# Kernel optimization log

Measured on AMD Instinct MI355X. Metric: run time of the kernel, lower is better.

Reference implementation:

```python
import jax, jax.numpy as jnp
import numpy as np

N = 50000       # nodes
E = 800000      # edges (avg degree 16)
IN = 256        # input feature dim
HID = 64        # per-head hidden dim
H = 2           # heads
C = 64          # num_classes (final single-head layer width)
NEG_SLOPE = 0.01  # torch F.leaky_relu default


def setup_inputs() -> dict:
    key = jax.random.key(0)
    ks = jax.random.split(key, 24)
    nrm = lambda k, shape, scale: jax.random.normal(k, shape, jnp.float32) * scale
    features = nrm(ks[0], (N, IN), 1.0)
    src = jax.random.randint(ks[1], (E,), 0, N)
    dst = jax.random.randint(ks[2], (E,), 0, N)
    # layer 0: H heads, Linear(IN->HID) + attn_l/attn_r Linear(HID->1)
    W0 = nrm(ks[3], (H, IN, HID), IN ** -0.5)
    b0 = jnp.zeros((H, HID), jnp.float32)
    al0 = nrm(ks[4], (H, HID), HID ** -0.5)
    bl0 = jnp.zeros((H,), jnp.float32)
    ar0 = nrm(ks[5], (H, HID), HID ** -0.5)
    br0 = jnp.zeros((H,), jnp.float32)
    # layer 1: H heads, Linear(H*HID->HID)
    W1 = nrm(ks[6], (H, H * HID, HID), (H * HID) ** -0.5)
    b1 = jnp.zeros((H, HID), jnp.float32)
    al1 = nrm(ks[7], (H, HID), HID ** -0.5)
    bl1 = jnp.zeros((H,), jnp.float32)
    ar1 = nrm(ks[8], (H, HID), HID ** -0.5)
    br1 = jnp.zeros((H,), jnp.float32)
    # final: 1 head, Linear(H*HID->C)
    Wf = nrm(ks[9], (1, H * HID, C), (H * HID) ** -0.5)
    bf = jnp.zeros((1, C), jnp.float32)
    alf = nrm(ks[10], (1, C), C ** -0.5)
    blf = jnp.zeros((1,), jnp.float32)
    arf = nrm(ks[11], (1, C), C ** -0.5)
    brf = jnp.zeros((1,), jnp.float32)
    return dict(features=features, src=src, dst=dst,
                W0=W0, b0=b0, al0=al0, bl0=bl0, ar0=ar0, br0=br0,
                W1=W1, b1=b1, al1=al1, bl1=bl1, ar1=ar1, br1=br1,
                Wf=Wf, bf=bf, alf=alf, blf=blf, arf=arf, brf=brf)


def gat_layer(x, src, dst, W, b, al, bl, ar, br):
    # x: [N, D]; W: [H, D, K]
    ft = jnp.einsum('nd,hdk->nhk', x, W) + b          # [N,H,K]
    a1 = jnp.einsum('nhk,hk->nh', ft, al) + bl        # [N,H] (dst-side)
    a2 = jnp.einsum('nhk,hk->nh', ft, ar) + br        # [N,H] (src-side)
    s = jax.nn.leaky_relu(a1[dst] + a2[src], NEG_SLOPE)  # [E,H]
    m = jax.ops.segment_max(s, dst, num_segments=N)      # per-dst max for stable softmax
    e = jnp.exp(s - m[dst])
    denom = jax.ops.segment_sum(e, dst, num_segments=N)
    alpha = e / denom[dst]                               # edge softmax over in-neighbors
    accum = jax.ops.segment_sum(alpha[:, :, None] * ft[src], dst, num_segments=N)  # [N,H,K]
    return jax.nn.elu(accum)


def reference(features, src, dst,
              W0, b0, al0, bl0, ar0, br0,
              W1, b1, al1, bl1, ar1, br1,
              Wf, bf, alf, blf, arf, brf):
    x = gat_layer(features, src, dst, W0, b0, al0, bl0, ar0, br0).reshape(N, H * HID)
    x = gat_layer(x, src, dst, W1, b1, al1, bl1, ar1, br1).reshape(N, H * HID)
    out = gat_layer(x, src, dst, Wf, bf, alf, blf, arf, brf)[:, 0, :]  # [N,C]
    return out
```

## Files before the change

### kernel.cpp

```cpp
#include <hip/hip_runtime.h>
#include <math.h>

#define NN 50000
#define EE 800000
#define DIN 256
#define NEG_SLOPE 0.01f
#define CAPSH 7
#define CAP (1 << CAPSH)

typedef __attribute__((ext_vector_type(8))) short bf16x8;
typedef __attribute__((ext_vector_type(8))) unsigned short u16x8;
typedef __attribute__((ext_vector_type(4))) float f32x4;

__device__ __forceinline__ unsigned short bf16_rne(float f) {
    unsigned int u = __float_as_uint(f);
    u += 0x7fffu + ((u >> 16) & 1u);
    return (unsigned short)(u >> 16);
}
__device__ __forceinline__ float bf16_tof(unsigned short h) {
    return __uint_as_float(((unsigned int)h) << 16);
}

__device__ __forceinline__ void fmamix_lo(float& a, unsigned f, float w) {
    asm("v_fma_mix_f32 %0, %1, %2, %0 op_sel:[0,0,0] op_sel_hi:[1,0,0]"
        : "+v"(a)
        : "v"(f), "v"(w));
}
__device__ __forceinline__ void fmamix_hi(float& a, unsigned f, float w) {
    asm("v_fma_mix_f32 %0, %1, %2, %0 op_sel:[1,0,0] op_sel_hi:[1,0,0]"
        : "+v"(a)
        : "v"(f), "v"(w));
}

__global__ __launch_bounds__(256) void scatter_kernel(const int* __restrict__ src,
                                                      const int* __restrict__ dst,
                                                      const int* __restrict__ pos,
                                                      int* __restrict__ esrc, int E) {
    int e = blockIdx.x * 256 + threadIdx.x;
    if (e >= E) return;
    int p = pos[e];
    if (p < CAP) esrc[(dst[e] << CAPSH) + p] = src[e];
}

__global__ __launch_bounds__(256) void conv_w_kernel(
    const float* __restrict__ W0, const float* __restrict__ W1,
    const float* __restrict__ Wf, unsigned short* __restrict__ w0h,
    unsigned short* __restrict__ w0l, unsigned short* __restrict__ w1h,
    unsigned short* __restrict__ w1l, unsigned short* __restrict__ wfh,
    unsigned short* __restrict__ wfl, int* __restrict__ cnt) {
    int t = blockIdx.x * 256 + threadIdx.x;
    const float* W;
    unsigned short *oh, *ol;
    int D, u;
    if (t < 32768) { W = W0; oh = w0h; ol = w0l; D = 256; u = t; }
    else if (t < 49152) { W = W1; oh = w1h; ol = w1l; D = 128; u = t - 32768; }
    else if (t < 57344) { W = Wf; oh = wfh; ol = wfl; D = 128; u = t - 49152; }
    else {
        int c = t - 57344;
        if (c < NN) cnt[c] = 0;
        return;
    }
    int d = u & (D - 1);
    int n = u / D;
    float v = W[((size_t)(n >> 6) * D + d) * 64 + (n & 63)];
    unsigned short hi = bf16_rne(v);
    unsigned short lo = bf16_rne(v - bf16_tof(hi));
    oh[(size_t)n * D + d] = hi;
    ol[(size_t)n * D + d] = lo;
}

#define LDK 40

template <int NCOL, bool AFP32, bool HIST>
__global__ __launch_bounds__(256) void gemm_attn(
    const float* __restrict__ Xf, const unsigned short* __restrict__ Xhi,
    const unsigned short* __restrict__ Xlo, const unsigned short* __restrict__ Wthi,
    const unsigned short* __restrict__ Wtlo, const float* __restrict__ bias,
    const float* __restrict__ al, const float* __restrict__ bl,
    const float* __restrict__ ar, const float* __restrict__ br,
    _Float16* __restrict__ FT, float* __restrict__ A1, float* __restrict__ A2,
    int Nn, int D, const int* __restrict__ edst, int* __restrict__ cnt,
    int* __restrict__ pos, int E, int gemmBlocks) {
    if (HIST) {
        if ((int)blockIdx.x >= gemmBlocks) {
            int e = ((int)blockIdx.x - gemmBlocks) * 256 + threadIdx.x;
            if (e < E) pos[e] = atomicAdd(&cnt[edst[e]], 1);
            return;
        }
    }
    const int H = NCOL / 64;
    const int NC16 = NCOL / 16;
    __shared__ __align__(16) unsigned short Ahi_s[64 * LDK];
    __shared__ __align__(16) unsigned short Alo_s[64 * LDK];
    __shared__ __align__(16) unsigned short Bhi_s[NCOL * LDK];
    __shared__ __align__(16) unsigned short Blo_s[NCOL * LDK];

    int tid = threadIdx.x;
    int wv = tid >> 6, l = tid & 63, lm = l & 15, quad = l >> 4;
    int m0 = blockIdx.x * 64;

    f32x4 acc[NC16];
#pragma unroll
    for (int c = 0; c < NC16; c++) acc[c] = (f32x4){0.f, 0.f, 0.f, 0.f};

    for (int d0 = 0; d0 < D; d0 += 32) {
        if (AFP32) {
#pragma unroll
            for (int i = 0; i < 2; i++) {
                int u = tid + i * 256;
                int row = u >> 3, c4 = u & 7;
                float4 v = make_float4(0.f, 0.f, 0.f, 0.f);
                if (m0 + row < Nn)
                    v = *(const float4*)&Xf[(size_t)(m0 + row) * D + d0 + c4 * 4];
                float f[4] = {v.x, v.y, v.z, v.w};
                unsigned short hi[4], lo[4];
#pragma unroll
                for (int j = 0; j < 4; j++) {
                    hi[j] = bf16_rne(f[j]);
                    lo[j] = bf16_rne(f[j] - bf16_tof(hi[j]));
                }
                *(ushort4*)&Ahi_s[row * LDK + c4 * 4] = make_ushort4(hi[0], hi[1], hi[2], hi[3]);
                *(ushort4*)&Alo_s[row * LDK + c4 * 4] = make_ushort4(lo[0], lo[1], lo[2], lo[3]);
            }
        } else {
            int row = tid >> 2, q = tid & 3;
            u16x8 vh = (u16x8)0, vl = (u16x8)0;
            if (m0 + row < Nn) {
                vh = *(const u16x8*)&Xhi[(size_t)(m0 + row) * D + d0 + q * 8];
                vl = *(const u16x8*)&Xlo[(size_t)(m0 + row) * D + d0 + q * 8];
            }
            *(u16x8*)&Ahi_s[row * LDK + q * 8] = vh;
            *(u16x8*)&Alo_s[row * LDK + q * 8] = vl;
        }
#pragma unroll
        for (int i = 0; i < NCOL / 64; i++) {
            int u = tid + i * 256;
            int n = u >> 2, q = u & 3;
            *(u16x8*)&Bhi_s[n * LDK + q * 8] =
                *(const u16x8*)&Wthi[(size_t)n * D + d0 + q * 8];
            *(u16x8*)&Blo_s[n * LDK + q * 8] =
                *(const u16x8*)&Wtlo[(size_t)n * D + d0 + q * 8];
        }
        __syncthreads();

        int arow = wv * 16 + lm;
        bf16x8 ah = *(const bf16x8*)&Ahi_s[arow * LDK + quad * 8];
        bf16x8 alo = *(const bf16x8*)&Alo_s[arow * LDK + quad * 8];
#pragma unroll
        for (int cg = 0; cg < NC16; cg += 4) {
            bf16x8 bh4[4], bl4[4];
#pragma unroll
            for (int u = 0; u < 4; u++) {
                bh4[u] = *(const bf16x8*)&Bhi_s[((cg + u) * 16 + lm) * LDK + quad * 8];
                bl4[u] = *(const bf16x8*)&Blo_s[((cg + u) * 16 + lm) * LDK + quad * 8];
            }
#pragma unroll
            for (int u = 0; u < 4; u++)
                acc[cg + u] = __builtin_amdgcn_mfma_f32_16x16x32_bf16(ah, bh4[u], acc[cg + u], 0, 0, 0);
#pragma unroll
            for (int u = 0; u < 4; u++)
                acc[cg + u] = __builtin_amdgcn_mfma_f32_16x16x32_bf16(ah, bl4[u], acc[cg + u], 0, 0, 0);
#pragma unroll
            for (int u = 0; u < 4; u++)
                acc[cg + u] = __builtin_amdgcn_mfma_f32_16x16x32_bf16(alo, bh4[u], acc[cg + u], 0, 0, 0);
        }
        __syncthreads();
    }

    float bj[NC16], alj[NC16], arj[NC16];
#pragma unroll
    for (int c = 0; c < NC16; c++) {
        bj[c] = bias[c * 16 + lm];
        alj[c] = al[c * 16 + lm];
        arj[c] = ar[c * 16 + lm];
    }
#pragma unroll
    for (int reg = 0; reg < 4; reg++) {
        int row = m0 + wv * 16 + quad * 4 + reg;
        bool ok = row < Nn;
        float s1[H], s2[H];
#pragma unroll
        for (int h = 0; h < H; h++) { s1[h] = 0.f; s2[h] = 0.f; }
#pragma unroll
        for (int c = 0; c < NC16; c++) {
            float o = acc[c][reg] + bj[c];
            int h = c >> 2;
            s1[h] += o * alj[c];
            s2[h] += o * arj[c];
            if (ok) FT[(size_t)row * NCOL + c * 16 + lm] = (_Float16)o;
        }
#pragma unroll
        for (int h = 0; h < H; h++) {
#pragma unroll
            for (int d = 1; d < 16; d <<= 1) {
                s1[h] += __shfl_xor(s1[h], d);
                s2[h] += __shfl_xor(s2[h], d);
            }
        }
        if (ok && lm == 0) {
#pragma unroll
            for (int h = 0; h < H; h++) {
                A1[(size_t)row * H + h] = s1[h] + bl[h];
                A2[(size_t)row * H + h] = s2[h] + br[h];
            }
        }
    }
}

__global__ __launch_bounds__(256) void agg2_kernel(
    const _Float16* __restrict__ ft, const float* __restrict__ a1,
    const float* __restrict__ a2, const int* __restrict__ cnt,
    const int* __restrict__ esrc, unsigned short* __restrict__ ohi,
    unsigned short* __restrict__ olo, int Nn) {
    __shared__ __align__(16) int2 pk0s[4][64];
    __shared__ __align__(16) int2 pk1s[4][64];
    int wv = threadIdx.x >> 6, lane = threadIdx.x & 63;
    int n = blockIdx.x * 4 + wv;
    if (n >= Nn) return;
    int o0 = n << CAPSH, deg = cnt[n];
    int hs = lane >> 5, cl2 = lane * 2;
    unsigned lb = (unsigned)lane * 4u;
    if (deg == 0) {
        *(ushort2*)&ohi[(size_t)n * 128 + cl2] = make_ushort2(0, 0);
        *(ushort2*)&olo[(size_t)n * 128 + cl2] = make_ushort2(0, 0);
        return;
    }
    const char* ftb = (const char*)ft;
    const int2* pw = hs ? pk1s[wv] : pk0s[wv];
    float2 a1v = *(const float2*)&a1[(size_t)n * 2];
    float ax = 0.f, ay = 0.f;
    float ds0 = 0.f, ds1 = 0.f;
    for (int e0 = 0; e0 < deg; e0 += 64) {
        int nE = min(64, deg - e0);
        float w0 = 0.f, w1 = 0.f;
        int sj = 0;
        if (lane < nE) {
            sj = esrc[o0 + e0 + lane];
            float2 a2j = *(const float2*)((const char*)a2 + ((unsigned)sj << 3));
            float t0 = a1v.x + a2j.x;
            float t1 = a1v.y + a2j.y;
            t0 = t0 > 0.f ? t0 : NEG_SLOPE * t0;
            t1 = t1 > 0.f ? t1 : NEG_SLOPE * t1;
            w0 = __expf(t0);
            w1 = __expf(t1);
        }
        ds0 += w0;
        ds1 += w1;
        pk0s[wv][lane] = make_int2(sj, __float_as_int(w0));
        pk1s[wv][lane] = make_int2(sj, __float_as_int(w1));
        int nB = (nE + 15) >> 4;
        for (int b = 0; b < nB; b++) {
            int j = b * 16;
            int2 pb[16];
#pragma unroll
            for (int u = 0; u < 16; u++) pb[u] = pw[j + u];
            unsigned f[16];
#pragma unroll
            for (int u = 0; u < 16; u++)
                f[u] = *(const unsigned*)(ftb + (((unsigned)pb[u].x << 8) + lb));
#pragma unroll
            for (int u = 0; u < 16; u++) {
                float w = __int_as_float(pb[u].y);
                fmamix_lo(ax, f[u], w);
                fmamix_hi(ay, f[u], w);
            }
        }
    }
#pragma unroll
    for (int d = 1; d < 64; d <<= 1) {
        ds0 += __shfl_xor(ds0, d);
        ds1 += __shfl_xor(ds1, d);
    }
    float rd = 1.f / (hs ? ds1 : ds0);
    float rx = ax * rd, ry = ay * rd;
    rx = rx > 0.f ? rx : expm1f(rx);
    ry = ry > 0.f ? ry : expm1f(ry);
    unsigned short hx = bf16_rne(rx), hy = bf16_rne(ry);
    unsigned short lx = bf16_rne(rx - bf16_tof(hx)), ly = bf16_rne(ry - bf16_tof(hy));
    *(ushort2*)&ohi[(size_t)n * 128 + cl2] = make_ushort2(hx, hy);
    *(ushort2*)&olo[(size_t)n * 128 + cl2] = make_ushort2(lx, ly);
}

__global__ __launch_bounds__(256) void agg1_kernel(
    const _Float16* __restrict__ ft, const float* __restrict__ a1,
    const float* __restrict__ a2, const int* __restrict__ cnt,
    const int* __restrict__ esrc, float* __restrict__ out, int Nn) {
    __shared__ __align__(16) int2 pks[4][64];
    int wv = threadIdx.x >> 6, lane = threadIdx.x & 63;
    int n = blockIdx.x * 4 + wv;
    if (n >= Nn) return;
    int o0 = n << CAPSH, deg = cnt[n];
    if (deg == 0) {
        out[(size_t)n * 64 + lane] = 0.f;
        return;
    }
    const char* ftb = (const char*)ft;
    unsigned lb = (unsigned)lane * 2u;
    float a1v = a1[n];
    float acc = 0.f, dsum = 0.f;
    for (int e0 = 0; e0 < deg; e0 += 64) {
        int nE = min(64, deg - e0);
        float wl = 0.f;
        int sj = 0;
        if (lane < nE) {
            sj = esrc[o0 + e0 + lane];
            float t = a1v + a2[sj];
            t = t > 0.f ? t : NEG_SLOPE * t;
            wl = __expf(t);
        }
        dsum += wl;
        pks[wv][lane] = make_int2(sj, __float_as_int(wl));
        int nB = (nE + 15) >> 4;
        for (int b = 0; b < nB; b++) {
            int j = b * 16;
            int2 pb[16];
#pragma unroll
            for (int u = 0; u < 16; u++) pb[u] = pks[wv][j + u];
            unsigned f[16];
#pragma unroll
            for (int u = 0; u < 16; u++)
                f[u] = *(const unsigned short*)(ftb + (((unsigned)pb[u].x << 7) + lb));
#pragma unroll
            for (int u = 0; u < 16; u++)
                fmamix_lo(acc, f[u], __int_as_float(pb[u].y));
        }
    }
#pragma unroll
    for (int d = 1; d < 64; d <<= 1) dsum += __shfl_xor(dsum, d);
    float r = acc / dsum;
    out[(size_t)n * 64 + lane] = r > 0.f ? r : expm1f(r);
}

extern "C" void kernel_launch(void* const* d_in, const int* in_sizes, int n_in,
                              void* d_out, int out_size, void* d_ws, size_t ws_size,
                              hipStream_t stream) {
    const float* features = (const float*)d_in[0];
    const int* src = (const int*)d_in[1];
    const int* dst = (const int*)d_in[2];
    const float* W0 = (const float*)d_in[3];
    const float* b0 = (const float*)d_in[4];
    const float* al0 = (const float*)d_in[5];
    const float* bl0 = (const float*)d_in[6];
    const float* ar0 = (const float*)d_in[7];
    const float* br0 = (const float*)d_in[8];
    const float* W1 = (const float*)d_in[9];
    const float* b1 = (const float*)d_in[10];
    const float* al1 = (const float*)d_in[11];
    const float* bl1 = (const float*)d_in[12];
    const float* ar1 = (const float*)d_in[13];
    const float* br1 = (const float*)d_in[14];
    const float* Wf = (const float*)d_in[15];
    const float* bf = (const float*)d_in[16];
    const float* alf = (const float*)d_in[17];
    const float* blf = (const float*)d_in[18];
    const float* arf = (const float*)d_in[19];
    const float* brf = (const float*)d_in[20];

    char* p = (char*)d_ws;
    auto carve = [&](size_t bytes) {
        void* q = (void*)p;
        p += (bytes + 255) & ~(size_t)255;
        return q;
    };
    _Float16* ft = (_Float16*)carve((size_t)NN * 128 * 2);
    unsigned short* Xhi = (unsigned short*)carve((size_t)NN * 128 * 2);
    unsigned short* Xlo = (unsigned short*)carve((size_t)NN * 128 * 2);
    float* a1 = (float*)carve((size_t)NN * 2 * 4);
    float* a2 = (float*)carve((size_t)NN * 2 * 4);
    int* cnt = (int*)carve((size_t)NN * 4);
    int* pos = (int*)carve((size_t)EE * 4);
    int* esrc = (int*)carve((size_t)NN * CAP * 4);
    unsigned short* w0h = (unsigned short*)carve(32768 * 2);
    unsigned short* w0l = (unsigned short*)carve(32768 * 2);
    unsigned short* w1h = (unsigned short*)carve(16384 * 2);
    unsigned short* w1l = (unsigned short*)carve(16384 * 2);
    unsigned short* wfh = (unsigned short*)carve(8192 * 2);
    unsigned short* wfl = (unsigned short*)carve(8192 * 2);

    const int GE = (EE + 255) / 256;
    const int gx = (NN + 63) / 64;
    const int gn = (NN + 3) / 4;

    conv_w_kernel<<<(57344 + NN + 255) / 256, 256, 0, stream>>>(
        W0, W1, Wf, w0h, w0l, w1h, w1l, wfh, wfl, cnt);

    gemm_attn<128, true, true><<<gx + GE, 256, 0, stream>>>(
        features, nullptr, nullptr, w0h, w0l, b0, al0, bl0, ar0, br0, ft, a1, a2,
        NN, DIN, dst, cnt, pos, EE, gx);

    scatter_kernel<<<GE, 256, 0, stream>>>(src, dst, pos, esrc, EE);

    agg2_kernel<<<gn, 256, 0, stream>>>(ft, a1, a2, cnt, esrc, Xhi, Xlo, NN);

    gemm_attn<128, false, false><<<gx, 256, 0, stream>>>(
        nullptr, Xhi, Xlo, w1h, w1l, b1, al1, bl1, ar1, br1, ft, a1, a2, NN, 128,
        nullptr, nullptr, nullptr, 0, 0);
    agg2_kernel<<<gn, 256, 0, stream>>>(ft, a1, a2, cnt, esrc, Xhi, Xlo, NN);

    gemm_attn<64, false, false><<<gx, 256, 0, stream>>>(
        nullptr, Xhi, Xlo, wfh, wfl, bf, alf, blf, arf, brf, ft, a1, a2, NN, 128,
        nullptr, nullptr, nullptr, 0, 0);
    agg1_kernel<<<gn, 256, 0, stream>>>(ft, a1, a2, cnt, esrc, (float*)d_out, NN);
}
```

Before: 292.0 us.

## Fuse edge aggregation with next layer GEMM, keeping aggregated tile in LDS

Merges the layer aggregation kernel with the following layer's projection GEMM. Each block aggregates 64 destination nodes into a swizzled LDS tile of bf16 hi/lo values, then multiplies that tile by the next weight matrix with MFMA. This removes the global write and re-read of the Xhi/Xlo intermediate and two kernel launches. Block count drops from one wave per node across many blocks to 64 nodes per block, which reduces parallelism and latency hiding for the irregular gather phase. Double-buffered ft/a1/a2 buffers are added to avoid read/write aliasing.

```diff
diff --git a/kernel.cpp b/kernel.cpp
--- a/kernel.cpp
+++ b/kernel.cpp
@@ -71,25 +71,20 @@
 
 #define LDK 40
 
-template <int NCOL, bool AFP32, bool HIST>
-__global__ __launch_bounds__(256) void gemm_attn(
-    const float* __restrict__ Xf, const unsigned short* __restrict__ Xhi,
-    const unsigned short* __restrict__ Xlo, const unsigned short* __restrict__ Wthi,
+__global__ __launch_bounds__(256) void gemm0_kernel(
+    const float* __restrict__ Xf, const unsigned short* __restrict__ Wthi,
     const unsigned short* __restrict__ Wtlo, const float* __restrict__ bias,
     const float* __restrict__ al, const float* __restrict__ bl,
     const float* __restrict__ ar, const float* __restrict__ br,
     _Float16* __restrict__ FT, float* __restrict__ A1, float* __restrict__ A2,
     int Nn, int D, const int* __restrict__ edst, int* __restrict__ cnt,
     int* __restrict__ pos, int E, int gemmBlocks) {
-    if (HIST) {
-        if ((int)blockIdx.x >= gemmBlocks) {
-            int e = ((int)blockIdx.x - gemmBlocks) * 256 + threadIdx.x;
-            if (e < E) pos[e] = atomicAdd(&cnt[edst[e]], 1);
-            return;
-        }
-    }
-    const int H = NCOL / 64;
-    const int NC16 = NCOL / 16;
+    if ((int)blockIdx.x >= gemmBlocks) {
+        int e = ((int)blockIdx.x - gemmBlocks) * 256 + threadIdx.x;
+        if (e < E) pos[e] = atomicAdd(&cnt[edst[e]], 1);
+        return;
+    }
+    const int NCOL = 128, NC16 = 8, H = 2;
     __shared__ __align__(16) unsigned short Ahi_s[64 * LDK];
     __shared__ __align__(16) unsigned short Alo_s[64 * LDK];
     __shared__ __align__(16) unsigned short Bhi_s[NCOL * LDK];
@@ -104,36 +99,25 @@
     for (int c = 0; c < NC16; c++) acc[c] = (f32x4){0.f, 0.f, 0.f, 0.f};
 
     for (int d0 = 0; d0 < D; d0 += 32) {
-        if (AFP32) {
-#pragma unroll
-            for (int i = 0; i < 2; i++) {
-                int u = tid + i * 256;
-                int row = u >> 3, c4 = u & 7;
-                float4 v = make_float4(0.f, 0.f, 0.f, 0.f);
-                if (m0 + row < Nn)
-                    v = *(const float4*)&Xf[(size_t)(m0 + row) * D + d0 + c4 * 4];
-                float f[4] = {v.x, v.y, v.z, v.w};
-                unsigned short hi[4], lo[4];
-#pragma unroll
-                for (int j = 0; j < 4; j++) {
-                    hi[j] = bf16_rne(f[j]);
-                    lo[j] = bf16_rne(f[j] - bf16_tof(hi[j]));
-                }
-                *(ushort4*)&Ahi_s[row * LDK + c4 * 4] = make_ushort4(hi[0], hi[1], hi[2], hi[3]);
-                *(ushort4*)&Alo_s[row * LDK + c4 * 4] = make_ushort4(lo[0], lo[1], lo[2], lo[3]);
-            }
-        } else {
-            int row = tid >> 2, q = tid & 3;
-            u16x8 vh = (u16x8)0, vl = (u16x8)0;
-            if (m0 + row < Nn) {
-                vh = *(const u16x8*)&Xhi[(size_t)(m0 + row) * D + d0 + q * 8];
-                vl = *(const u16x8*)&Xlo[(size_t)(m0 + row) * D + d0 + q * 8];
-            }
-            *(u16x8*)&Ahi_s[row * LDK + q * 8] = vh;
-            *(u16x8*)&Alo_s[row * LDK + q * 8] = vl;
-        }
-#pragma unroll
-        for (int i = 0; i < NCOL / 64; i++) {
+#pragma unroll
+        for (int i = 0; i < 2; i++) {
+            int u = tid + i * 256;
+            int row = u >> 3, c4 = u & 7;
+            float4 v = make_float4(0.f, 0.f, 0.f, 0.f);
+            if (m0 + row < Nn)
+                v = *(const float4*)&Xf[(size_t)(m0 + row) * D + d0 + c4 * 4];
+            float f[4] = {v.x, v.y, v.z, v.w};
+            unsigned short hi[4], lo[4];
+#pragma unroll
+            for (int j = 0; j < 4; j++) {
+                hi[j] = bf16_rne(f[j]);
+                lo[j] = bf16_rne(f[j] - bf16_tof(hi[j]));
+            }
+            *(ushort4*)&Ahi_s[row * LDK + c4 * 4] = make_ushort4(hi[0], hi[1], hi[2], hi[3]);
+            *(ushort4*)&Alo_s[row * LDK + c4 * 4] = make_ushort4(lo[0], lo[1], lo[2], lo[3]);
+        }
+#pragma unroll
+        for (int i = 0; i < 2; i++) {
             int u = tid + i * 256;
             int n = u >> 2, q = u & 3;
             *(u16x8*)&Bhi_s[n * LDK + q * 8] =
@@ -207,78 +191,181 @@
     }
 }
 
-__global__ __launch_bounds__(256) void agg2_kernel(
-    const _Float16* __restrict__ ft, const float* __restrict__ a1,
-    const float* __restrict__ a2, const int* __restrict__ cnt,
-    const int* __restrict__ esrc, unsigned short* __restrict__ ohi,
-    unsigned short* __restrict__ olo, int Nn) {
-    __shared__ __align__(16) int2 pk0s[4][64];
-    __shared__ __align__(16) int2 pk1s[4][64];
-    int wv = threadIdx.x >> 6, lane = threadIdx.x & 63;
-    int n = blockIdx.x * 4 + wv;
-    if (n >= Nn) return;
-    int o0 = n << CAPSH, deg = cnt[n];
-    int hs = lane >> 5, cl2 = lane * 2;
-    unsigned lb = (unsigned)lane * 4u;
-    if (deg == 0) {
-        *(ushort2*)&ohi[(size_t)n * 128 + cl2] = make_ushort2(0, 0);
-        *(ushort2*)&olo[(size_t)n * 128 + cl2] = make_ushort2(0, 0);
-        return;
-    }
-    const char* ftb = (const char*)ft;
-    const int2* pw = hs ? pk1s[wv] : pk0s[wv];
-    float2 a1v = *(const float2*)&a1[(size_t)n * 2];
-    float ax = 0.f, ay = 0.f;
-    float ds0 = 0.f, ds1 = 0.f;
-    for (int e0 = 0; e0 < deg; e0 += 64) {
-        int nE = min(64, deg - e0);
-        float w0 = 0.f, w1 = 0.f;
-        int sj = 0;
-        if (lane < nE) {
-            sj = esrc[o0 + e0 + lane];
-            float2 a2j = *(const float2*)((const char*)a2 + ((unsigned)sj << 3));
-            float t0 = a1v.x + a2j.x;
-            float t1 = a1v.y + a2j.y;
-            t0 = t0 > 0.f ? t0 : NEG_SLOPE * t0;
-            t1 = t1 > 0.f ? t1 : NEG_SLOPE * t1;
-            w0 = __expf(t0);
-            w1 = __expf(t1);
-        }
-        ds0 += w0;
-        ds1 += w1;
-        pk0s[wv][lane] = make_int2(sj, __float_as_int(w0));
-        pk1s[wv][lane] = make_int2(sj, __float_as_int(w1));
-        int nB = (nE + 15) >> 4;
-        for (int b = 0; b < nB; b++) {
-            int j = b * 16;
-            int2 pb[16];
-#pragma unroll
-            for (int u = 0; u < 16; u++) pb[u] = pw[j + u];
-            unsigned f[16];
-#pragma unroll
-            for (int u = 0; u < 16; u++)
-                f[u] = *(const unsigned*)(ftb + (((unsigned)pb[u].x << 8) + lb));
-#pragma unroll
-            for (int u = 0; u < 16; u++) {
-                float w = __int_as_float(pb[u].y);
-                fmamix_lo(ax, f[u], w);
-                fmamix_hi(ay, f[u], w);
-            }
-        }
-    }
-#pragma unroll
-    for (int d = 1; d < 64; d <<= 1) {
-        ds0 += __shfl_xor(ds0, d);
-        ds1 += __shfl_xor(ds1, d);
-    }
-    float rd = 1.f / (hs ? ds1 : ds0);
-    float rx = ax * rd, ry = ay * rd;
-    rx = rx > 0.f ? rx : expm1f(rx);
-    ry = ry > 0.f ? ry : expm1f(ry);
-    unsigned short hx = bf16_rne(rx), hy = bf16_rne(ry);
-    unsigned short lx = bf16_rne(rx - bf16_tof(hx)), ly = bf16_rne(ry - bf16_tof(hy));
-    *(ushort2*)&ohi[(size_t)n * 128 + cl2] = make_ushort2(hx, hy);
-    *(ushort2*)&olo[(size_t)n * 128 + cl2] = make_ushort2(lx, ly);
+template <int NCOL>
+__global__ __launch_bounds__(256) void agg_gemm_kernel(
+    const _Float16* __restrict__ ftin, const float* __restrict__ a1in,
+    const float* __restrict__ a2in, const int* __restrict__ cnt,
+    const int* __restrict__ esrc, const unsigned short* __restrict__ Wthi,
+    const unsigned short* __restrict__ Wtlo, const float* __restrict__ bias,
+    const float* __restrict__ al, const float* __restrict__ bl,
+    const float* __restrict__ ar, const float* __restrict__ br,
+    _Float16* __restrict__ FT, float* __restrict__ A1, float* __restrict__ A2,
+    int Nn) {
+    const int NC16 = NCOL / 16;
+    const int H = NCOL / 64;
+    __shared__ __align__(16) unsigned short Ahi_t[64 * 128];
+    __shared__ __align__(16) unsigned short Alo_t[64 * 128];
+    __shared__ __align__(16) unsigned short Bhi_s[64 * LDK];
+    __shared__ __align__(16) unsigned short Blo_s[64 * LDK];
+    int2* pk0s = (int2*)Bhi_s;
+    int2* pk1s = (int2*)Blo_s;
+
+    int tid = threadIdx.x;
+    int wv = tid >> 6, lane = tid & 63, lm = lane & 15, quad = lane >> 4;
+    int m0 = blockIdx.x * 64;
+    const char* ftb = (const char*)ftin;
+
+    {
+        int hs = lane >> 5;
+        unsigned lb = (unsigned)lane * 4u;
+        const int2* pw = (hs ? pk1s : pk0s) + wv * 64;
+        for (int i = 0; i < 16; i++) {
+            int r = wv * 16 + i;
+            int n = m0 + r;
+            unsigned abyte = ((unsigned)(r * 256 + lane * 4)) ^ ((unsigned)(r & 7) << 4);
+            if (n >= Nn) {
+                *(ushort2*)((char*)Ahi_t + abyte) = make_ushort2(0, 0);
+                *(ushort2*)((char*)Alo_t + abyte) = make_ushort2(0, 0);
+                continue;
+            }
+            int deg = cnt[n];
+            if (deg == 0) {
+                *(ushort2*)((char*)Ahi_t + abyte) = make_ushort2(0, 0);
+                *(ushort2*)((char*)Alo_t + abyte) = make_ushort2(0, 0);
+                continue;
+            }
+            int o0 = n << CAPSH;
+            float2 a1v = *(const float2*)&a1in[(size_t)n * 2];
+            float ax = 0.f, ay = 0.f, ds0 = 0.f, ds1 = 0.f;
+            for (int e0 = 0; e0 < deg; e0 += 64) {
+                int nE = min(64, deg - e0);
+                float w0 = 0.f, w1 = 0.f;
+                int sj = 0;
+                if (lane < nE) {
+                    sj = esrc[o0 + e0 + lane];
+                    float2 a2j = *(const float2*)((const char*)a2in + ((unsigned)sj << 3));
+                    float t0 = a1v.x + a2j.x;
+                    float t1 = a1v.y + a2j.y;
+                    t0 = t0 > 0.f ? t0 : NEG_SLOPE * t0;
+                    t1 = t1 > 0.f ? t1 : NEG_SLOPE * t1;
+                    w0 = __expf(t0);
+                    w1 = __expf(t1);
+                }
+                ds0 += w0;
+                ds1 += w1;
+                pk0s[wv * 64 + lane] = make_int2(sj, __float_as_int(w0));
+                pk1s[wv * 64 + lane] = make_int2(sj, __float_as_int(w1));
+                int nB = (nE + 15) >> 4;
+                for (int b = 0; b < nB; b++) {
+                    int j = b * 16;
+                    int2 pb[16];
+#pragma unroll
+                    for (int u = 0; u < 16; u++) pb[u] = pw[j + u];
+                    unsigned f[16];
+#pragma unroll
+                    for (int u = 0; u < 16; u++)
+                        f[u] = *(const unsigned*)(ftb + (((unsigned)pb[u].x << 8) + lb));
+#pragma unroll
+                    for (int u = 0; u < 16; u++) {
+                        float w = __int_as_float(pb[u].y);
+                        fmamix_lo(ax, f[u], w);
+                        fmamix_hi(ay, f[u], w);
+                    }
+                }
+            }
+#pragma unroll
+            for (int d = 1; d < 64; d <<= 1) {
+                ds0 += __shfl_xor(ds0, d);
+                ds1 += __shfl_xor(ds1, d);
+            }
+            float rd = 1.f / (hs ? ds1 : ds0);
+            float rx = ax * rd, ry = ay * rd;
+            rx = rx > 0.f ? rx : expm1f(rx);
+            ry = ry > 0.f ? ry : expm1f(ry);
+            unsigned short hx = bf16_rne(rx), hy = bf16_rne(ry);
+            unsigned short lx = bf16_rne(rx - bf16_tof(hx)), ly = bf16_rne(ry - bf16_tof(hy));
+            *(ushort2*)((char*)Ahi_t + abyte) = make_ushort2(hx, hy);
+            *(ushort2*)((char*)Alo_t + abyte) = make_ushort2(lx, ly);
+        }
+    }
+    __syncthreads();
+
+    f32x4 acc[NC16];
+#pragma unroll
+    for (int c = 0; c < NC16; c++) acc[c] = (f32x4){0.f, 0.f, 0.f, 0.f};
+
+    int arow = wv * 16 + lm;
+    for (int d0 = 0; d0 < 128; d0 += 32) {
+#pragma unroll
+        for (int h = 0; h < NCOL / 64; h++) {
+            int bn = tid >> 2, q = tid & 3;
+            *(u16x8*)&Bhi_s[bn * LDK + q * 8] =
+                *(const u16x8*)&Wthi[(size_t)(h * 64 + bn) * 128 + d0 + q * 8];
+            *(u16x8*)&Blo_s[bn * LDK + q * 8] =
+                *(const u16x8*)&Wtlo[(size_t)(h * 64 + bn) * 128 + d0 + q * 8];
+            __syncthreads();
+
+            unsigned ab = ((unsigned)(arow * 256 + (d0 + quad * 8) * 2)) ^
+                          ((unsigned)(arow & 7) << 4);
+            bf16x8 ah = *(const bf16x8*)((const char*)Ahi_t + ab);
+            bf16x8 alo = *(const bf16x8*)((const char*)Alo_t + ab);
+            bf16x8 bh4[4], bl4[4];
+#pragma unroll
+            for (int u = 0; u < 4; u++) {
+                bh4[u] = *(const bf16x8*)&Bhi_s[(u * 16 + lm) * LDK + quad * 8];
+                bl4[u] = *(const bf16x8*)&Blo_s[(u * 16 + lm) * LDK + quad * 8];
+            }
+#pragma unroll
+            for (int u = 0; u < 4; u++)
+                acc[h * 4 + u] = __builtin_amdgcn_mfma_f32_16x16x32_bf16(ah, bh4[u], acc[h * 4 + u], 0, 0, 0);
+#pragma unroll
+            for (int u = 0; u < 4; u++)
+                acc[h * 4 + u] = __builtin_amdgcn_mfma_f32_16x16x32_bf16(ah, bl4[u], acc[h * 4 + u], 0, 0, 0);
+#pragma unroll
+            for (int u = 0; u < 4; u++)
+                acc[h * 4 + u] = __builtin_amdgcn_mfma_f32_16x16x32_bf16(alo, bh4[u], acc[h * 4 + u], 0, 0, 0);
+            __syncthreads();
+        }
+    }
+
+    float bj[NC16], alj[NC16], arj[NC16];
+#pragma unroll
+    for (int c = 0; c < NC16; c++) {
+        bj[c] = bias[c * 16 + lm];
+        alj[c] = al[c * 16 + lm];
+        arj[c] = ar[c * 16 + lm];
+    }
+#pragma unroll
+    for (int reg = 0; reg < 4; reg++) {
+        int row = m0 + wv * 16 + quad * 4 + reg;
+        bool ok = row < Nn;
+        float s1[H], s2[H];
+#pragma unroll
+        for (int h = 0; h < H; h++) { s1[h] = 0.f; s2[h] = 0.f; }
+#pragma unroll
+        for (int c = 0; c < NC16; c++) {
+            float o = acc[c][reg] + bj[c];
+            int h = c >> 2;
+            s1[h] += o * alj[c];
+            s2[h] += o * arj[c];
+            if (ok) FT[(size_t)row * NCOL + c * 16 + lm] = (_Float16)o;
+        }
+#pragma unroll
+        for (int h = 0; h < H; h++) {
+#pragma unroll
+            for (int d = 1; d < 16; d <<= 1) {
+                s1[h] += __shfl_xor(s1[h], d);
+                s2[h] += __shfl_xor(s2[h], d);
+            }
+        }
+        if (ok && lm == 0) {
+#pragma unroll
+            for (int h = 0; h < H; h++) {
+                A1[(size_t)row * H + h] = s1[h] + bl[h];
+                A2[(size_t)row * H + h] = s2[h] + br[h];
+            }
+        }
+    }
 }
 
 __global__ __launch_bounds__(256) void agg1_kernel(
@@ -362,11 +449,12 @@
         p += (bytes + 255) & ~(size_t)255;
         return q;
     };
-    _Float16* ft = (_Float16*)carve((size_t)NN * 128 * 2);
-    unsigned short* Xhi = (unsigned short*)carve((size_t)NN * 128 * 2);
-    unsigned short* Xlo = (unsigned short*)carve((size_t)NN * 128 * 2);
-    float* a1 = (float*)carve((size_t)NN * 2 * 4);
-    float* a2 = (float*)carve((size_t)NN * 2 * 4);
+    _Float16* ftA = (_Float16*)carve((size_t)NN * 128 * 2);
+    _Float16* ftB = (_Float16*)carve((size_t)NN * 128 * 2);
+    float* a1A = (float*)carve((size_t)NN * 2 * 4);
+    float* a2A = (float*)carve((size_t)NN * 2 * 4);
+    float* a1B = (float*)carve((size_t)NN * 2 * 4);
+    float* a2B = (float*)carve((size_t)NN * 2 * 4);
     int* cnt = (int*)carve((size_t)NN * 4);
     int* pos = (int*)carve((size_t)EE * 4);
     int* esrc = (int*)carve((size_t)NN * CAP * 4);
@@ -384,21 +472,19 @@
     conv_w_kernel<<<(57344 + NN + 255) / 256, 256, 0, stream>>>(
         W0, W1, Wf, w0h, w0l, w1h, w1l, wfh, wfl, cnt);
 
-    gemm_attn<128, true, true><<<gx + GE, 256, 0, stream>>>(
-        features, nullptr, nullptr, w0h, w0l, b0, al0, bl0, ar0, br0, ft, a1, a2,
+    gemm0_kernel<<<gx + GE, 256, 0, stream>>>(
+        features, w0h, w0l, b0, al0, bl0, ar0, br0, ftA, a1A, a2A,
         NN, DIN, dst, cnt, pos, EE, gx);
 
     scatter_kernel<<<GE, 256, 0, stream>>>(src, dst, pos, esrc, EE);
 
-    agg2_kernel<<<gn, 256, 0, stream>>>(ft, a1, a2, cnt, esrc, Xhi, Xlo, NN);
-
-    gemm_attn<128, false, false><<<gx, 256, 0, stream>>>(
-        nullptr, Xhi, Xlo, w1h, w1l, b1, al1, bl1, ar1, br1, ft, a1, a2, NN, 128,
-        nullptr, nullptr, nullptr, 0, 0);
-    agg2_kernel<<<gn, 256, 0, stream>>>(ft, a1, a2, cnt, esrc, Xhi, Xlo, NN);
-
-    gemm_attn<64, false, false><<<gx, 256, 0, stream>>>(
-        nullptr, Xhi, Xlo, wfh, wfl, bf, alf, blf, arf, brf, ft, a1, a2, NN, 128,
-        nullptr, nullptr, nullptr, 0, 0);
-    agg1_kernel<<<gn, 256, 0, stream>>>(ft, a1, a2, cnt, esrc, (float*)d_out, NN);
-}
+    agg_gemm_kernel<128><<<gx, 256, 0, stream>>>(
+        ftA, a1A, a2A, cnt, esrc, w1h, w1l, b1, al1, bl1, ar1, br1,
+        ftB, a1B, a2B, NN);
+
+    agg_gemm_kernel<64><<<gx, 256, 0, stream>>>(
+        ftB, a1B, a2B, cnt, esrc, wfh, wfl, bf, alf, blf, arf, brf,
+        ftA, a1A, a2A, NN);
+
+    agg1_kernel<<<gn, 256, 0, stream>>>(ftA, a1A, a2A, cnt, esrc, (float*)d_out, NN);
+}
```

Result: slower. 358.7 us (+22.8%).
